# Performance work log

Measured on AMD Instinct MI355X. Metric: run time of the kernel, lower is better.

The kernel has to match this reference:

```python
import jax, jax.numpy as jnp
import numpy as np

B, S, HID = 4, 2048, 2048
NH, NKV, D = 16, 8, 128
RK, RV = 16, 16
HPG = NH // NKV
SCALING = D ** -0.5
NEG = -1e9


def _rope(x, cos, sin):
    # x: [B, S, H, D]; cos/sin: [S, D//2]. Gemma split-half complex rotation.
    x1, x2 = jnp.split(x, 2, axis=-1)
    c = cos[None, :, None, :]
    s = sin[None, :, None, :]
    return jnp.concatenate([x1 * c - x2 * s, x1 * s + x2 * c], axis=-1)


def setup_inputs() -> dict:
    key = jax.random.key(0)
    ks = jax.random.split(key, 8)
    hidden_states = jax.random.normal(ks[0], (B, S, HID), dtype=jnp.float32)
    # RoPE frequencies (theta=10000)
    inv_freq = 1.0 / (10000.0 ** (np.arange(0, D, 2, dtype=np.float32) / D))
    ang = np.arange(S, dtype=np.float32)[:, None] * inv_freq[None, :]
    freqs_cos = jnp.asarray(np.cos(ang), dtype=jnp.float32)
    freqs_sin = jnp.asarray(np.sin(ang), dtype=jnp.float32)
    kv_write_indices = jnp.arange(S, dtype=jnp.int32)
    # causal additive mask [1,1,S,S]
    causal = jnp.tril(jnp.ones((S, S), dtype=bool))
    mask = jnp.where(causal, 0.0, NEG).astype(jnp.float32)[None, None]
    sc = 0.02
    W_q = jax.random.normal(ks[1], (NH * D, HID), dtype=jnp.float32) * sc
    W_k = jax.random.normal(ks[2], (NKV * D, HID), dtype=jnp.float32) * sc
    W_v = jax.random.normal(ks[3], (NKV * D, HID), dtype=jnp.float32) * sc
    o_proj_w = jax.random.normal(ks[4], (HID, NH * D), dtype=jnp.float32) * sc
    V_r_basis = jax.random.normal(ks[5], (NH, D, RK), dtype=jnp.float32) * (D ** -0.5)
    Z_v_basis = jax.random.normal(ks[6], (NKV, D, RV), dtype=jnp.float32) * (D ** -0.5)
    return {"hidden_states": hidden_states, "freqs_cos": freqs_cos, "freqs_sin": freqs_sin,
            "kv_write_indices": kv_write_indices, "mask": mask, "W_q": W_q, "W_k": W_k,
            "W_v": W_v, "o_proj_w": o_proj_w, "V_r_basis": V_r_basis, "Z_v_basis": Z_v_basis}


def reference(hidden_states, freqs_cos, freqs_sin, kv_write_indices, mask,
              W_q, W_k, W_v, o_proj_w, V_r_basis, Z_v_basis):
    bsz, q_len, _ = hidden_states.shape
    q = (hidden_states @ W_q.T).reshape(bsz, q_len, NH, D)
    k = (hidden_states @ W_k.T).reshape(bsz, q_len, NKV, D)
    v = (hidden_states @ W_v.T).reshape(bsz, q_len, NKV, D)

    # project K per-head onto its group's basis (vectorized over the head loop)
    head_to_group = jnp.arange(NH) // HPG                       # [NH]
    k_per_head = k[:, :, head_to_group, :]                      # [B,S,NH,D]
    pk = jnp.einsum('bshd,hdr->bshr', k_per_head, V_r_basis)    # [B,S,NH,RK]
    pv = jnp.einsum('bqgd,gdr->bqgr', v, Z_v_basis)             # [B,S,NKV,RV]

    # factorized cache write (scatter along seq dim), prefill: kv_seq_len = S
    kv_seq_len = q_len
    cache_pk = jnp.zeros((bsz, kv_seq_len, NH, RK), hidden_states.dtype)
    cache_pv = jnp.zeros((bsz, kv_seq_len, NKV, RV), hidden_states.dtype)
    cache_pk = cache_pk.at[:, kv_write_indices].set(pk)
    cache_pv = cache_pv.at[:, kv_write_indices].set(pv)

    # reconstruct K/V from compressed cache
    k_hat = jnp.einsum('bshr,hrd->bshd', cache_pk, jnp.swapaxes(V_r_basis, -1, -2))
    v_hat = jnp.einsum('bsgr,grd->bsgd', cache_pv, jnp.swapaxes(Z_v_basis, -1, -2))

    # RoPE post-reconstruction
    q_rot = _rope(q, freqs_cos[:q_len], freqs_sin[:q_len])
    k_rot = _rope(k_hat, freqs_cos[:kv_seq_len], freqs_sin[:kv_seq_len])

    # GQA: repeat kv heads
    v_g = jnp.repeat(v_hat, HPG, axis=2)                        # [B,S,NH,D]

    scores = jnp.einsum('bqhd,bkhd->bhqk', q_rot, k_rot) * SCALING
    scores = scores + mask[:, :, :q_len, :kv_seq_len]
    probs = jax.nn.softmax(scores.astype(jnp.float32), axis=-1).astype(hidden_states.dtype)
    out = jnp.einsum('bhqk,bkhd->bqhd', probs, v_g)
    out = out.reshape(bsz, q_len, NH * D)
    return out @ o_proj_w.T
```

## Files before the change

kernel.cpp:

```cpp
#include <hip/hip_runtime.h>

typedef unsigned short ushort8 __attribute__((ext_vector_type(8)));
typedef short s16x8 __attribute__((ext_vector_type(8)));
typedef float f32x4 __attribute__((ext_vector_type(4)));

#define AS1 __attribute__((address_space(1)))
#define AS3 __attribute__((address_space(3)))

#define B_    4
#define S_    2048
#define HID_  2048
#define NH_   16
#define NKV_  8
#define D_    128
#define RK_   16
#define SCALING_ 0.08838834764831845f
#define LOG2E_   1.4426950408889634f
#define NEGBIG   -1.0e30f

__device__ __forceinline__ float bf2f(unsigned short u) {
  union { unsigned int i; float f; } x; x.i = ((unsigned int)u) << 16; return x.f;
}
__device__ __forceinline__ unsigned short f2bf(float f) {
  union { float f; unsigned int i; } x; x.f = f;
  unsigned int r = x.i + 0x7fffu + ((x.i >> 16) & 1u);
  return (unsigned short)(r >> 16);
}

__global__ __launch_bounds__(256) void cvt_bf16(const float* __restrict__ in,
                                                unsigned short* __restrict__ out,
                                                int n8) {
  int i = blockIdx.x * 256 + threadIdx.x;
  const int stride = gridDim.x * 256;
  for (; i < n8; i += stride) {
    const float4 a = ((const float4*)in)[i * 2];
    const float4 b = ((const float4*)in)[i * 2 + 1];
    ushort8 u;
    u[0] = f2bf(a.x); u[1] = f2bf(a.y); u[2] = f2bf(a.z); u[3] = f2bf(a.w);
    u[4] = f2bf(b.x); u[5] = f2bf(b.y); u[6] = f2bf(b.z); u[7] = f2bf(b.w);
    *(ushort8*)&out[i * 8] = u;
  }
}

template<bool CBF>
__global__ __launch_bounds__(256) void gemm_mfma(const unsigned short* __restrict__ A,
                                                 const unsigned short* __restrict__ Bb,
                                                 void* __restrict__ C_,
                                                 int M, int N, int K) {
  __shared__ unsigned short Ash[128 * 64];
  __shared__ unsigned short Bsh[128 * 64];
  const int tid = threadIdx.x;
  const int w = tid >> 6, l = tid & 63, lg = l >> 4, ll = l & 15;
  const int wr = w >> 1, wc = w & 1;
  const int flat = blockIdx.y * gridDim.x + blockIdx.x;
  const int cpx = (gridDim.x * gridDim.y) >> 3;
  const int swz = (flat & 7) * cpx + (flat >> 3);
  const int bm = (swz / gridDim.x) * 128, bn = (swz % gridDim.x) * 128;

  f32x4 acc[4][4];
#pragma unroll
  for (int i = 0; i < 4; i++)
#pragma unroll
    for (int j = 0; j < 4; j++) acc[i][j] = (f32x4){0.f, 0.f, 0.f, 0.f};

  const int srow = tid >> 3;
  const int sslot = tid & 7;

  for (int k0 = 0; k0 < K; k0 += 64) {
    __syncthreads();
#pragma unroll
    for (int c = 0; c < 4; ++c) {
      const int row = c * 32 + srow;
      const int ss = sslot ^ (row & 7);
      const unsigned short* srcA = &A[(size_t)(bm + row) * K + k0 + ss * 8];
      const unsigned short* srcB = &Bb[(size_t)(bn + row) * K + k0 + ss * 8];
      char* dstA = ((char*)Ash) + c * 4096 + w * 1024;
      char* dstB = ((char*)Bsh) + c * 4096 + w * 1024;
      __builtin_amdgcn_global_load_lds((const AS1 void*)srcA, (AS3 void*)dstA, 16, 0, 0);
      __builtin_amdgcn_global_load_lds((const AS1 void*)srcB, (AS3 void*)dstB, 16, 0, 0);
    }
    __syncthreads();

#pragma unroll
    for (int ks = 0; ks < 2; ++ks) {
      s16x8 af[4], bf_[4];
#pragma unroll
      for (int mi = 0; mi < 4; ++mi) {
        const int row = wr * 64 + mi * 16 + ll;
        af[mi] = *(const s16x8*)&Ash[row * 64 + (((ks * 4 + lg) ^ (row & 7)) * 8)];
      }
#pragma unroll
      for (int ni = 0; ni < 4; ++ni) {
        const int row = wc * 64 + ni * 16 + ll;
        bf_[ni] = *(const s16x8*)&Bsh[row * 64 + (((ks * 4 + lg) ^ (row & 7)) * 8)];
      }
#pragma unroll
      for (int mi = 0; mi < 4; ++mi)
#pragma unroll
        for (int ni = 0; ni < 4; ++ni)
          acc[mi][ni] = __builtin_amdgcn_mfma_f32_16x16x32_bf16(af[mi], bf_[ni], acc[mi][ni], 0, 0, 0);
    }
  }

#pragma unroll
  for (int mi = 0; mi < 4; ++mi)
#pragma unroll
    for (int ni = 0; ni < 4; ++ni)
#pragma unroll
      for (int j = 0; j < 4; ++j) {
        const int row = bm + wr * 64 + mi * 16 + lg * 4 + j;
        const int col = bn + wc * 64 + ni * 16 + ll;
        if (CBF) ((unsigned short*)C_)[(size_t)row * N + col] = f2bf(acc[mi][ni][j]);
        else     ((float*)C_)[(size_t)row * N + col] = acc[mi][ni][j];
      }
}

__global__ __launch_bounds__(256) void rope_q(unsigned short* __restrict__ q,
                                              const float* __restrict__ cosT,
                                              const float* __restrict__ sinT) {
  const int p = blockIdx.x * 256 + threadIdx.x;
  const int d = p & 63;
  const int h = (p >> 6) & 15;
  const int s = (p >> 10) & 2047;
  const int b = p >> 21;
  const size_t base = (((size_t)b * S_ + s) * NH_ + h) * D_ + d;
  const float x1 = bf2f(q[base]), x2 = bf2f(q[base + 64]);
  const float c = cosT[s * 64 + d], sn = sinT[s * 64 + d];
  const float sc = SCALING_ * LOG2E_;
  q[base]      = f2bf((x1 * c - x2 * sn) * sc);
  q[base + 64] = f2bf((x1 * sn + x2 * c) * sc);
}

__global__ __launch_bounds__(256) void pkpv_make(const unsigned short* __restrict__ kv_raw,
                                                 const float* __restrict__ Vr,
                                                 const float* __restrict__ Zv,
                                                 float* __restrict__ pk,
                                                 float* __restrict__ pv) {
  const int s = blockIdx.x, b = blockIdx.y;
  const int tid = threadIdx.x;
  __shared__ float kb[NKV_ * D_];
  __shared__ float vb[NKV_ * D_];
  {
    const size_t o = ((size_t)b * S_ + s) * 2048;
    ushort4 ku = *(const ushort4*)&kv_raw[o + tid * 4];
    kb[tid * 4 + 0] = bf2f(ku.x); kb[tid * 4 + 1] = bf2f(ku.y);
    kb[tid * 4 + 2] = bf2f(ku.z); kb[tid * 4 + 3] = bf2f(ku.w);
    ushort4 vu = *(const ushort4*)&kv_raw[o + 1024 + tid * 4];
    vb[tid * 4 + 0] = bf2f(vu.x); vb[tid * 4 + 1] = bf2f(vu.y);
    vb[tid * 4 + 2] = bf2f(vu.z); vb[tid * 4 + 3] = bf2f(vu.w);
  }
  __syncthreads();
  {
    const int h = tid >> 4, r = tid & 15, g = h >> 1;
    float a = 0.f;
    const float* vr = &Vr[(size_t)h * D_ * RK_ + r];
    const float* kk = &kb[g * D_];
#pragma unroll 8
    for (int d = 0; d < D_; d++) a += kk[d] * vr[d * RK_];
    pk[(((size_t)b * S_ + s) * NH_ + h) * RK_ + r] = a;
  }
  if (tid < 128) {
    const int g = tid >> 4, r = tid & 15;
    float a = 0.f;
    const float* zv = &Zv[(size_t)g * D_ * RK_ + r];
    const float* vv = &vb[g * D_];
#pragma unroll 8
    for (int d = 0; d < D_; d++) a += vv[d] * zv[d * RK_];
    pv[(((size_t)b * S_ + s) * NKV_ + g) * RK_ + r] = a;
  }
}

__global__ __launch_bounds__(256) void expand_k(const float* __restrict__ pk,
                                                const float* __restrict__ Vr,
                                                const float* __restrict__ cosT,
                                                const float* __restrict__ sinT,
                                                unsigned short* __restrict__ kr) {
  const int s0 = blockIdx.x * 32, h = blockIdx.y, b = blockIdx.z;
  const int tid = threadIdx.x;
  __shared__ float pkS[32][17];
  if (tid < 128) {
    const int r_ = tid >> 2, c4 = (tid & 3) * 4;
    float4 v = *(const float4*)&pk[(((size_t)b * S_ + s0 + r_) * NH_ + h) * RK_ + c4];
    pkS[r_][c4 + 0] = v.x; pkS[r_][c4 + 1] = v.y;
    pkS[r_][c4 + 2] = v.z; pkS[r_][c4 + 3] = v.w;
  }
  __syncthreads();
  const int row = tid >> 3, dl = tid & 7;
  float kh[16];
#pragma unroll
  for (int j = 0; j < 16; j++) {
    const int d = dl + 8 * j;
    const float4* w = (const float4*)&Vr[((size_t)h * D_ + d) * RK_];
    float a = 0.f;
#pragma unroll
    for (int q4 = 0; q4 < 4; q4++) {
      float4 wv = w[q4];
      a += pkS[row][q4 * 4 + 0] * wv.x + pkS[row][q4 * 4 + 1] * wv.y
         + pkS[row][q4 * 4 + 2] * wv.z + pkS[row][q4 * 4 + 3] * wv.w;
    }
    kh[j] = a;
  }
  const int pos = s0 + row;
  const size_t o = (((size_t)b * NH_ + h) * S_ + pos) * D_;
#pragma unroll
  for (int j = 0; j < 8; j++) {
    const int d = dl + 8 * j;
    const float c = cosT[pos * 64 + d], sn = sinT[pos * 64 + d];
    kr[o + d]      = f2bf(kh[j] * c - kh[j + 8] * sn);
    kr[o + d + 64] = f2bf(kh[j] * sn + kh[j + 8] * c);
  }
}

__global__ __launch_bounds__(256) void expand_v(const float* __restrict__ pv,
                                                const float* __restrict__ Zv,
                                                unsigned short* __restrict__ vh) {
  const int s0 = blockIdx.x * 32, g = blockIdx.y, b = blockIdx.z;
  const int tid = threadIdx.x;
  __shared__ float pvS[32][17];
  if (tid < 128) {
    const int r_ = tid >> 2, c4 = (tid & 3) * 4;
    float4 v = *(const float4*)&pv[(((size_t)b * S_ + s0 + r_) * NKV_ + g) * RK_ + c4];
    pvS[r_][c4 + 0] = v.x; pvS[r_][c4 + 1] = v.y;
    pvS[r_][c4 + 2] = v.z; pvS[r_][c4 + 3] = v.w;
  }
  __syncthreads();
  const int row = tid >> 3, dl = tid & 7;
  const size_t o = (((size_t)b * NKV_ + g) * S_ + s0 + row) * D_;
#pragma unroll
  for (int j = 0; j < 16; j++) {
    const int d = dl + 8 * j;
    const float4* w = (const float4*)&Zv[((size_t)g * D_ + d) * RK_];
    float a = 0.f;
#pragma unroll
    for (int q4 = 0; q4 < 4; q4++) {
      float4 wv = w[q4];
      a += pvS[row][q4 * 4 + 0] * wv.x + pvS[row][q4 * 4 + 1] * wv.y
         + pvS[row][q4 * 4 + 2] * wv.z + pvS[row][q4 * 4 + 3] * wv.w;
    }
    vh[o + d] = f2bf(a);
  }
}

__global__ __launch_bounds__(256) void attn_mfma(const unsigned short* __restrict__ q,
                                                 const unsigned short* __restrict__ kr,
                                                 const unsigned short* __restrict__ vh,
                                                 unsigned short* __restrict__ out) {
  const int flat = ((int)blockIdx.z * 16 + (int)blockIdx.y) * 16 + (int)blockIdx.x;
  const int swz = (flat & 7) * 128 + (flat >> 3);
  const int qt = 15 - (swz & 15);
  const int h = (swz >> 4) & 15;
  const int b = swz >> 8;
  const int g = h >> 1;
  const int tid = threadIdx.x;
  const int w = tid >> 6, l = tid & 63, lg = l >> 4, ll = l & 15;

  __shared__ unsigned short Klds[2][64 * 128];
  __shared__ unsigned short Vt[2][128 * 64];
  __shared__ unsigned short Ps[4][32 * 64];

  const int qr0 = qt * 128 + w * 32;
  const int ktmax = 2 * qt + 1;
  const int kmy = 2 * qt + (w >> 1);

  s16x8 qf[2][4];
#pragma unroll
  for (int mi = 0; mi < 2; ++mi)
#pragma unroll
    for (int ks = 0; ks < 4; ++ks)
      qf[mi][ks] = *(const s16x8*)&q[(((size_t)b * S_ + qr0 + mi * 16 + ll) * NH_ + h) * D_ + ks * 32 + lg * 8];

  f32x4 o[2][8];
#pragma unroll
  for (int mi = 0; mi < 2; ++mi)
#pragma unroll
    for (int nd = 0; nd < 8; ++nd) o[mi][nd] = (f32x4){0.f, 0.f, 0.f, 0.f};
  float m_[2][4], l_[2][4];
#pragma unroll
  for (int mi = 0; mi < 2; ++mi)
#pragma unroll
    for (int j = 0; j < 4; ++j) { m_[mi][j] = NEGBIG; l_[mi][j] = 0.f; }

  const unsigned short* kbase = &kr[(((size_t)b * NH_ + h) * S_) * D_];
  const unsigned short* vbase = &vh[(((size_t)b * NKV_ + g) * S_) * D_];
  const int vk = (tid & 31) * 2, d0v = (tid >> 5) * 16;

  ushort8 va0, va1, vb0, vb1;
  {
#pragma unroll
    for (int c = 0; c < 4; ++c) {
      const int ro = c * 16 + w * 4 + lg;
      const int ss = ll ^ (ro & 7);
      const unsigned short* src = kbase + ro * D_ + ss * 8;
      char* dst = ((char*)&Klds[0][0]) + c * 4096 + w * 1024;
      __builtin_amdgcn_global_load_lds((const AS1 void*)src, (AS3 void*)dst, 16, 0, 0);
    }
    const unsigned short* v0 = vbase + (size_t)vk * D_ + d0v;
    va0 = *(const ushort8*)v0; va1 = *(const ushort8*)(v0 + 8);
    vb0 = *(const ushort8*)(v0 + D_); vb1 = *(const ushort8*)(v0 + D_ + 8);
#pragma unroll
    for (int j = 0; j < 8; ++j) {
      const int d1 = d0v + j, d2 = d0v + 8 + j;
      *(unsigned int*)&Vt[0][d1 * 64 + (((vk >> 3) ^ (d1 & 7)) * 8) + (vk & 7)] =
          (unsigned int)va0[j] | ((unsigned int)vb0[j] << 16);
      *(unsigned int*)&Vt[0][d2 * 64 + (((vk >> 3) ^ (d2 & 7)) * 8) + (vk & 7)] =
          (unsigned int)va1[j] | ((unsigned int)vb1[j] << 16);
    }
  }
  __syncthreads();

  for (int kt = 0; kt <= ktmax; ++kt) {
    const int p = kt & 1;
    if (kt < ktmax) {
      const unsigned short* kb2 = kbase + (size_t)(kt + 1) * 64 * D_;
#pragma unroll
      for (int c = 0; c < 4; ++c) {
        const int ro = c * 16 + w * 4 + lg;
        const int ss = ll ^ (ro & 7);
        const unsigned short* src = kb2 + ro * D_ + ss * 8;
        char* dst = ((char*)&Klds[p ^ 1][0]) + c * 4096 + w * 1024;
        __builtin_amdgcn_global_load_lds((const AS1 void*)src, (AS3 void*)dst, 16, 0, 0);
      }
      const unsigned short* v0 = vbase + (size_t)((kt + 1) * 64 + vk) * D_ + d0v;
      va0 = *(const ushort8*)v0; va1 = *(const ushort8*)(v0 + 8);
      vb0 = *(const ushort8*)(v0 + D_); vb1 = *(const ushort8*)(v0 + D_ + 8);
    }

    if (kt <= kmy) {
      f32x4 s[2][4];
#pragma unroll
      for (int mi = 0; mi < 2; ++mi)
#pragma unroll
        for (int ni = 0; ni < 4; ++ni) s[mi][ni] = (f32x4){0.f, 0.f, 0.f, 0.f};
      __builtin_amdgcn_s_setprio(1);
#pragma unroll
      for (int ks = 0; ks < 4; ++ks) {
#pragma unroll
        for (int ni = 0; ni < 4; ++ni) {
          const int row = ni * 16 + ll;
          const s16x8 kf = *(const s16x8*)&Klds[p][row * 128 + (((ks * 4 + lg) ^ (row & 7)) * 8)];
          s[0][ni] = __builtin_amdgcn_mfma_f32_16x16x32_bf16(qf[0][ks], kf, s[0][ni], 0, 0, 0);
          s[1][ni] = __builtin_amdgcn_mfma_f32_16x16x32_bf16(qf[1][ks], kf, s[1][ni], 0, 0, 0);
        }
      }
      __builtin_amdgcn_s_setprio(0);

      const bool diag = (kt == kmy);
      float lm[2][4];
#pragma unroll
      for (int mi = 0; mi < 2; ++mi)
#pragma unroll
        for (int j = 0; j < 4; ++j) {
          if (diag) {
            const int qg = qr0 + mi * 16 + lg * 4 + j;
#pragma unroll
            for (int ni = 0; ni < 4; ++ni)
              if (kt * 64 + ni * 16 + ll > qg) s[mi][ni][j] = NEGBIG;
          }
          lm[mi][j] = fmaxf(fmaxf(s[mi][0][j], s[mi][1][j]),
                            fmaxf(s[mi][2][j], s[mi][3][j]));
        }
      float excess = lm[0][0] - m_[0][0];
#pragma unroll
      for (int mi = 0; mi < 2; ++mi)
#pragma unroll
        for (int j = 0; j < 4; ++j) excess = fmaxf(excess, lm[mi][j] - m_[mi][j]);
      const bool slow = __any(excess > 11.5f);

#pragma unroll
      for (int mi = 0; mi < 2; ++mi)
#pragma unroll
        for (int j = 0; j < 4; ++j) {
          float ps_[4];
          if (slow) {
            float mt = lm[mi][j];
            mt = fmaxf(mt, __shfl_xor(mt, 1));
            mt = fmaxf(mt, __shfl_xor(mt, 2));
            mt = fmaxf(mt, __shfl_xor(mt, 4));
            mt = fmaxf(mt, __shfl_xor(mt, 8));
            const float mnew = fmaxf(m_[mi][j], mt);
            const float al = exp2f(m_[mi][j] - mnew);
            m_[mi][j] = mnew;
            float sum = 0.f;
#pragma unroll
            for (int ni = 0; ni < 4; ++ni) { ps_[ni] = exp2f(s[mi][ni][j] - mnew); sum += ps_[ni]; }
            l_[mi][j] = l_[mi][j] * al + sum;
#pragma unroll
            for (int nd = 0; nd < 8; ++nd) o[mi][nd][j] *= al;
          } else {
            float sum = 0.f;
#pragma unroll
            for (int ni = 0; ni < 4; ++ni) { ps_[ni] = exp2f(s[mi][ni][j] - m_[mi][j]); sum += ps_[ni]; }
            l_[mi][j] += sum;
          }
          const int prow = mi * 16 + lg * 4 + j;
#pragma unroll
          for (int nq = 0; nq < 2; ++nq) {
            unsigned int u;
            asm("v_cvt_pk_bf16_f32 %0, %1, %2" : "=v"(u) : "v"(ps_[nq * 2]), "v"(ps_[nq * 2 + 1]));
            const int c0 = nq * 32 + ll, c1 = nq * 32 + 16 + ll;
            Ps[w][prow * 64 + (((c0 >> 3) ^ (prow & 7)) * 8) + (ll & 7)] = (unsigned short)u;
            Ps[w][prow * 64 + (((c1 >> 3) ^ (prow & 7)) * 8) + (ll & 7)] = (unsigned short)(u >> 16);
          }
        }

      s16x8 pa[2][2];
#pragma unroll
      for (int mi = 0; mi < 2; ++mi)
#pragma unroll
        for (int ks2 = 0; ks2 < 2; ++ks2) {
          const int prow = mi * 16 + ll;
          pa[mi][ks2] = *(const s16x8*)&Ps[w][prow * 64 + (((ks2 * 4 + lg) ^ (prow & 7)) * 8)];
        }
      __builtin_amdgcn_s_setprio(1);
#pragma unroll
      for (int nd = 0; nd < 8; ++nd) {
#pragma unroll
        for (int ks2 = 0; ks2 < 2; ++ks2) {
          const int vr = nd * 16 + ll;
          const s16x8 vbf = *(const s16x8*)&Vt[p][vr * 64 + (((ks2 * 4 + lg) ^ (vr & 7)) * 8)];
          o[0][nd] = __builtin_amdgcn_mfma_f32_16x16x32_bf16(pa[0][ks2], vbf, o[0][nd], 0, 0, 0);
          o[1][nd] = __builtin_amdgcn_mfma_f32_16x16x32_bf16(pa[1][ks2], vbf, o[1][nd], 0, 0, 0);
        }
      }
      __builtin_amdgcn_s_setprio(0);
    }

    if (kt < ktmax) {
#pragma unroll
      for (int j = 0; j < 8; ++j) {
        const int d1 = d0v + j, d2 = d0v + 8 + j;
        *(unsigned int*)&Vt[p ^ 1][d1 * 64 + (((vk >> 3) ^ (d1 & 7)) * 8) + (vk & 7)] =
            (unsigned int)va0[j] | ((unsigned int)vb0[j] << 16);
        *(unsigned int*)&Vt[p ^ 1][d2 * 64 + (((vk >> 3) ^ (d2 & 7)) * 8) + (vk & 7)] =
            (unsigned int)va1[j] | ((unsigned int)vb1[j] << 16);
      }
    }
    __syncthreads();
  }

#pragma unroll
  for (int mi = 0; mi < 2; ++mi)
#pragma unroll
    for (int j = 0; j < 4; ++j) {
      float ls = l_[mi][j];
      ls += __shfl_xor(ls, 1);
      ls += __shfl_xor(ls, 2);
      ls += __shfl_xor(ls, 4);
      ls += __shfl_xor(ls, 8);
      const float inv = 1.f / ls;
      const size_t rowg = (size_t)b * S_ + qr0 + mi * 16 + lg * 4 + j;
      unsigned short* op = &out[rowg * (NH_ * D_) + h * D_ + ll];
#pragma unroll
      for (int nd = 0; nd < 8; ++nd) op[nd * 16] = f2bf(o[mi][nd][j] * inv);
    }
}

extern "C" void kernel_launch(void* const* d_in, const int* in_sizes, int n_in,
                              void* d_out, int out_size, void* d_ws, size_t ws_size,
                              hipStream_t stream) {
  const float* hidden = (const float*)d_in[0];
  const float* cosT   = (const float*)d_in[1];
  const float* sinT   = (const float*)d_in[2];
  const float* W_q    = (const float*)d_in[5];
  const float* W_k    = (const float*)d_in[6];
  const float* W_v    = (const float*)d_in[7];
  const float* W_o    = (const float*)d_in[8];
  const float* Vr     = (const float*)d_in[9];
  const float* Zv     = (const float*)d_in[10];
  float* out = (float*)d_out;

  char* ws = (char*)d_ws;
  unsigned short* hb     = (unsigned short*)(ws + 0);
  unsigned short* attn_b = (unsigned short*)(ws + 0);
  unsigned short* q_b    = (unsigned short*)(ws + 33554432);
  unsigned short* kv_b   = (unsigned short*)(ws + 67108864);
  unsigned short* kr_b   = (unsigned short*)(ws + 67108864);
  unsigned short* vh_b   = (unsigned short*)(ws + 100663296);
  unsigned short* Wkv    = (unsigned short*)(ws + 100663296);
  unsigned short* WR1    = (unsigned short*)(ws + 117440512);
  float*          pk_f   = (float*)(ws + 117440512);
  float*          pv_f   = (float*)(ws + 125829120);

  const int M = B_ * S_;

  cvt_bf16<<<2048, 256, 0, stream>>>(hidden, hb, (B_ * S_ * HID_) / 8);
  cvt_bf16<<<2048, 256, 0, stream>>>(W_q, WR1, (HID_ * HID_) / 8);
  cvt_bf16<<<1024, 256, 0, stream>>>(W_k, Wkv, (NKV_ * D_ * HID_) / 8);
  cvt_bf16<<<1024, 256, 0, stream>>>(W_v, Wkv + (size_t)NKV_ * D_ * HID_, (NKV_ * D_ * HID_) / 8);

  gemm_mfma<true><<<dim3(16, 64), 256, 0, stream>>>(hb, WR1, q_b,  M, 2048, HID_);
  gemm_mfma<true><<<dim3(16, 64), 256, 0, stream>>>(hb, Wkv, kv_b, M, 2048, HID_);

  rope_q<<<(B_ * S_ * NH_ * 64) / 256, 256, 0, stream>>>(q_b, cosT, sinT);

  pkpv_make<<<dim3(S_, B_), 256, 0, stream>>>(kv_b, Vr, Zv, pk_f, pv_f);

  expand_k<<<dim3(S_ / 32, NH_, B_), 256, 0, stream>>>(pk_f, Vr, cosT, sinT, kr_b);
  expand_v<<<dim3(S_ / 32, NKV_, B_), 256, 0, stream>>>(pv_f, Zv, vh_b);

  cvt_bf16<<<2048, 256, 0, stream>>>(W_o, WR1, (HID_ * HID_) / 8);

  attn_mfma<<<dim3(16, 16, 4), 256, 0, stream>>>(q_b, kr_b, vh_b, attn_b);

  gemm_mfma<false><<<dim3(16, 64), 256, 0, stream>>>(attn_b, WR1, out, M, HID_, HID_);
}
```

Before: 860.1 us.

## Fold K/V low-rank bases into projection weights and drop setprio in attention

Precomputes fused weights W_k^T·V_r and W_v^T·Z_v (384 output rows) in a new kernel, so hidden states are projected straight to the compressed pk/pv with one small GEMM. This replaces the full 2048-wide K/V GEMM, two weight conversions and the pkpv_make kernel. It also removes the s_setprio calls around the MFMA blocks in attention. The fused weights are rounded to bf16 after the product, which changes rounding slightly. The 3-wide GEMM grid also gives lower occupancy for that GEMM.

```diff
diff --git a/kernel.cpp b/kernel.cpp
--- a/kernel.cpp
+++ b/kernel.cpp
@@ -40,6 +40,40 @@
     u[4] = f2bf(b.x); u[5] = f2bf(b.y); u[6] = f2bf(b.z); u[7] = f2bf(b.w);
     *(ushort8*)&out[i * 8] = u;
   }
+}
+
+__global__ __launch_bounds__(256) void wfuse(const float* __restrict__ W_k,
+                                             const float* __restrict__ W_v,
+                                             const float* __restrict__ Vr,
+                                             const float* __restrict__ Zv,
+                                             unsigned short* __restrict__ Wf) {
+  const int idx = blockIdx.x;
+  const int cc = blockIdx.y * 256;
+  const int tid = threadIdx.x;
+  const bool isK = idx < 16;
+  const int hg = isK ? idx : (idx - 16);
+  const int wrow0 = isK ? (idx * 16) : (256 + (idx - 16) * 16);
+  const float* W = isK ? &W_k[(size_t)((hg >> 1) * 128) * HID_]
+                       : &W_v[(size_t)(hg * 128) * HID_];
+  const float* P = isK ? &Vr[(size_t)hg * 128 * 16] : &Zv[(size_t)hg * 128 * 16];
+  __shared__ float Wl[32][257];
+  float acc[16] = {};
+  for (int d0 = 0; d0 < 128; d0 += 32) {
+    __syncthreads();
+#pragma unroll 8
+    for (int dd = 0; dd < 32; ++dd)
+      Wl[dd][tid] = W[(size_t)(d0 + dd) * HID_ + cc + tid];
+    __syncthreads();
+#pragma unroll 8
+    for (int dd = 0; dd < 32; ++dd) {
+      const float w = Wl[dd][tid];
+#pragma unroll
+      for (int r = 0; r < 16; ++r) acc[r] += w * P[(d0 + dd) * 16 + r];
+    }
+  }
+#pragma unroll
+  for (int r = 0; r < 16; ++r)
+    Wf[(size_t)(wrow0 + r) * HID_ + cc + tid] = f2bf(acc[r]);
 }
 
 template<bool CBF>
@@ -131,46 +165,7 @@
   q[base + 64] = f2bf((x1 * sn + x2 * c) * sc);
 }
 
-__global__ __launch_bounds__(256) void pkpv_make(const unsigned short* __restrict__ kv_raw,
-                                                 const float* __restrict__ Vr,
-                                                 const float* __restrict__ Zv,
-                                                 float* __restrict__ pk,
-                                                 float* __restrict__ pv) {
-  const int s = blockIdx.x, b = blockIdx.y;
-  const int tid = threadIdx.x;
-  __shared__ float kb[NKV_ * D_];
-  __shared__ float vb[NKV_ * D_];
-  {
-    const size_t o = ((size_t)b * S_ + s) * 2048;
-    ushort4 ku = *(const ushort4*)&kv_raw[o + tid * 4];
-    kb[tid * 4 + 0] = bf2f(ku.x); kb[tid * 4 + 1] = bf2f(ku.y);
-    kb[tid * 4 + 2] = bf2f(ku.z); kb[tid * 4 + 3] = bf2f(ku.w);
-    ushort4 vu = *(const ushort4*)&kv_raw[o + 1024 + tid * 4];
-    vb[tid * 4 + 0] = bf2f(vu.x); vb[tid * 4 + 1] = bf2f(vu.y);
-    vb[tid * 4 + 2] = bf2f(vu.z); vb[tid * 4 + 3] = bf2f(vu.w);
-  }
-  __syncthreads();
-  {
-    const int h = tid >> 4, r = tid & 15, g = h >> 1;
-    float a = 0.f;
-    const float* vr = &Vr[(size_t)h * D_ * RK_ + r];
-    const float* kk = &kb[g * D_];
-#pragma unroll 8
-    for (int d = 0; d < D_; d++) a += kk[d] * vr[d * RK_];
-    pk[(((size_t)b * S_ + s) * NH_ + h) * RK_ + r] = a;
-  }
-  if (tid < 128) {
-    const int g = tid >> 4, r = tid & 15;
-    float a = 0.f;
-    const float* zv = &Zv[(size_t)g * D_ * RK_ + r];
-    const float* vv = &vb[g * D_];
-#pragma unroll 8
-    for (int d = 0; d < D_; d++) a += vv[d] * zv[d * RK_];
-    pv[(((size_t)b * S_ + s) * NKV_ + g) * RK_ + r] = a;
-  }
-}
-
-__global__ __launch_bounds__(256) void expand_k(const float* __restrict__ pk,
+__global__ __launch_bounds__(256) void expand_k(const float* __restrict__ pkpv,
                                                 const float* __restrict__ Vr,
                                                 const float* __restrict__ cosT,
                                                 const float* __restrict__ sinT,
@@ -180,7 +175,7 @@
   __shared__ float pkS[32][17];
   if (tid < 128) {
     const int r_ = tid >> 2, c4 = (tid & 3) * 4;
-    float4 v = *(const float4*)&pk[(((size_t)b * S_ + s0 + r_) * NH_ + h) * RK_ + c4];
+    float4 v = *(const float4*)&pkpv[(size_t)(b * S_ + s0 + r_) * 384 + h * 16 + c4];
     pkS[r_][c4 + 0] = v.x; pkS[r_][c4 + 1] = v.y;
     pkS[r_][c4 + 2] = v.z; pkS[r_][c4 + 3] = v.w;
   }
@@ -211,7 +206,7 @@
   }
 }
 
-__global__ __launch_bounds__(256) void expand_v(const float* __restrict__ pv,
+__global__ __launch_bounds__(256) void expand_v(const float* __restrict__ pkpv,
                                                 const float* __restrict__ Zv,
                                                 unsigned short* __restrict__ vh) {
   const int s0 = blockIdx.x * 32, g = blockIdx.y, b = blockIdx.z;
@@ -219,7 +214,7 @@
   __shared__ float pvS[32][17];
   if (tid < 128) {
     const int r_ = tid >> 2, c4 = (tid & 3) * 4;
-    float4 v = *(const float4*)&pv[(((size_t)b * S_ + s0 + r_) * NKV_ + g) * RK_ + c4];
+    float4 v = *(const float4*)&pkpv[(size_t)(b * S_ + s0 + r_) * 384 + 256 + g * 16 + c4];
     pvS[r_][c4 + 0] = v.x; pvS[r_][c4 + 1] = v.y;
     pvS[r_][c4 + 2] = v.z; pvS[r_][c4 + 3] = v.w;
   }
@@ -331,7 +326,6 @@
       for (int mi = 0; mi < 2; ++mi)
 #pragma unroll
         for (int ni = 0; ni < 4; ++ni) s[mi][ni] = (f32x4){0.f, 0.f, 0.f, 0.f};
-      __builtin_amdgcn_s_setprio(1);
 #pragma unroll
       for (int ks = 0; ks < 4; ++ks) {
 #pragma unroll
@@ -342,7 +336,6 @@
           s[1][ni] = __builtin_amdgcn_mfma_f32_16x16x32_bf16(qf[1][ks], kf, s[1][ni], 0, 0, 0);
         }
       }
-      __builtin_amdgcn_s_setprio(0);
 
       const bool diag = (kt == kmy);
       float lm[2][4];
@@ -411,7 +404,6 @@
           const int prow = mi * 16 + ll;
           pa[mi][ks2] = *(const s16x8*)&Ps[w][prow * 64 + (((ks2 * 4 + lg) ^ (prow & 7)) * 8)];
         }
-      __builtin_amdgcn_s_setprio(1);
 #pragma unroll
       for (int nd = 0; nd < 8; ++nd) {
 #pragma unroll
@@ -422,7 +414,6 @@
           o[1][nd] = __builtin_amdgcn_mfma_f32_16x16x32_bf16(pa[1][ks2], vbf, o[1][nd], 0, 0, 0);
         }
       }
-      __builtin_amdgcn_s_setprio(0);
     }
 
     if (kt < ktmax) {
@@ -473,30 +464,25 @@
   unsigned short* hb     = (unsigned short*)(ws + 0);
   unsigned short* attn_b = (unsigned short*)(ws + 0);
   unsigned short* q_b    = (unsigned short*)(ws + 33554432);
-  unsigned short* kv_b   = (unsigned short*)(ws + 67108864);
   unsigned short* kr_b   = (unsigned short*)(ws + 67108864);
+  unsigned short* Wf     = (unsigned short*)(ws + 100663296);
   unsigned short* vh_b   = (unsigned short*)(ws + 100663296);
-  unsigned short* Wkv    = (unsigned short*)(ws + 100663296);
   unsigned short* WR1    = (unsigned short*)(ws + 117440512);
-  float*          pk_f   = (float*)(ws + 117440512);
-  float*          pv_f   = (float*)(ws + 125829120);
+  float*          pkpv   = (float*)(ws + 117440512);
 
   const int M = B_ * S_;
 
   cvt_bf16<<<2048, 256, 0, stream>>>(hidden, hb, (B_ * S_ * HID_) / 8);
   cvt_bf16<<<2048, 256, 0, stream>>>(W_q, WR1, (HID_ * HID_) / 8);
-  cvt_bf16<<<1024, 256, 0, stream>>>(W_k, Wkv, (NKV_ * D_ * HID_) / 8);
-  cvt_bf16<<<1024, 256, 0, stream>>>(W_v, Wkv + (size_t)NKV_ * D_ * HID_, (NKV_ * D_ * HID_) / 8);
-
-  gemm_mfma<true><<<dim3(16, 64), 256, 0, stream>>>(hb, WR1, q_b,  M, 2048, HID_);
-  gemm_mfma<true><<<dim3(16, 64), 256, 0, stream>>>(hb, Wkv, kv_b, M, 2048, HID_);
+  gemm_mfma<true><<<dim3(16, 64), 256, 0, stream>>>(hb, WR1, q_b, M, 2048, HID_);
+
+  wfuse<<<dim3(24, 8), 256, 0, stream>>>(W_k, W_v, Vr, Zv, Wf);
+  gemm_mfma<false><<<dim3(3, 64), 256, 0, stream>>>(hb, Wf, pkpv, M, 384, HID_);
 
   rope_q<<<(B_ * S_ * NH_ * 64) / 256, 256, 0, stream>>>(q_b, cosT, sinT);
 
-  pkpv_make<<<dim3(S_, B_), 256, 0, stream>>>(kv_b, Vr, Zv, pk_f, pv_f);
-
-  expand_k<<<dim3(S_ / 32, NH_, B_), 256, 0, stream>>>(pk_f, Vr, cosT, sinT, kr_b);
-  expand_v<<<dim3(S_ / 32, NKV_, B_), 256, 0, stream>>>(pv_f, Zv, vh_b);
+  expand_k<<<dim3(S_ / 32, NH_, B_), 256, 0, stream>>>(pkpv, Vr, cosT, sinT, kr_b);
+  expand_v<<<dim3(S_ / 32, NKV_, B_), 256, 0, stream>>>(pkpv, Zv, vh_b);
 
   cvt_bf16<<<2048, 256, 0, stream>>>(W_o, WR1, (HID_ * HID_) / 8);
 
```

New measurement: 752.4 us. 12.5% less time.
